# Optimization experiments

Measured on AMD Instinct MI355X. Metric: run time of the kernel, lower is better.

Reference implementation:

```python
import jax, jax.numpy as jnp
import numpy as np

D_MODEL = 1024
HEADS = 16
D_K = D_MODEL // HEADS  # 64


def setup_inputs() -> dict:
    key = jax.random.key(0)
    ks = jax.random.split(key, 9)
    B, S = 4, 2048
    values = jax.random.normal(ks[0], (B, S, D_MODEL), dtype=jnp.float32)
    keys = jax.random.normal(ks[1], (B, S, D_MODEL), dtype=jnp.float32)
    query = jax.random.normal(ks[2], (B, S, D_MODEL), dtype=jnp.float32)
    mask = jax.random.randint(ks[3], (1, 1, S, S), 0, 2, dtype=jnp.int32)
    # per-head projection weights (shared across heads), torch Linear layout (out, in)
    sc = 1.0 / np.sqrt(D_K)
    Wv = jax.random.uniform(ks[4], (D_K, D_K), jnp.float32, -sc, sc)
    Wk = jax.random.uniform(ks[5], (D_K, D_K), jnp.float32, -sc, sc)
    Wq = jax.random.uniform(ks[6], (D_K, D_K), jnp.float32, -sc, sc)
    so = 1.0 / np.sqrt(D_MODEL)
    Wo = jax.random.uniform(ks[7], (D_MODEL, D_MODEL), jnp.float32, -so, so)
    bo = jax.random.uniform(ks[8], (D_MODEL,), jnp.float32, -so, so)
    return {"values": values, "keys": keys, "query": query, "mask": mask,
            "Wv": Wv, "Wk": Wk, "Wq": Wq, "Wo": Wo, "bo": bo}


def reference(values, keys, query, mask, Wv, Wk, Wq, Wo, bo):
    n, q_len, d = query.shape
    v_len, k_len = values.shape[1], keys.shape[1]
    # reshape to (n, len, heads, d_k) and apply shared per-head linear (x @ W^T)
    v = values.reshape(n, v_len, HEADS, D_K) @ Wv.T
    k = keys.reshape(n, k_len, HEADS, D_K) @ Wk.T
    q = query.reshape(n, q_len, HEADS, D_K) @ Wq.T
    # scores: (n, h, q, k)
    scores = jnp.einsum('nqhd,nkhd->nhqk', q, k)
    scores = jnp.where(mask == 0, jnp.float32(-1e20), scores)
    attn = jax.nn.softmax(scores / jnp.sqrt(jnp.float32(D_K)), axis=3)
    out = jnp.einsum('nhqk,nkhd->nqhd', attn, v).reshape(n, q_len, HEADS * D_K)
    return out @ Wo.T + bo
```

## Files before the change

kernel.cpp:

```cpp
#include <hip/hip_runtime.h>

#define B 4
#define S 2048
#define H 16
#define DK 64
#define DM 1024
#define NTILES (S / 64)
#define QSCALE 0.18033688011112042f

typedef _Float16 half_t;
typedef __attribute__((ext_vector_type(8))) _Float16 half8v;
typedef __attribute__((ext_vector_type(2))) __fp16   fp16x2;
typedef __attribute__((ext_vector_type(4))) float    float4v;

__device__ __forceinline__ unsigned pkh(float lo, float hi) {
    union { fp16x2 h; unsigned u; } cvt;
    cvt.h = __builtin_amdgcn_cvt_pkrtz(lo, hi);
    return cvt.u;
}
__device__ __forceinline__ float fast_exp2(float x) {
#if __has_builtin(__builtin_amdgcn_exp2f)
    return __builtin_amdgcn_exp2f(x);
#else
    return __expf(x * 0.69314718055994531f);
#endif
}
__device__ __forceinline__ half8v cvt8h(float4 a, float4 b) {
    half8v r;
    r[0] = (half_t)a.x; r[1] = (half_t)a.y; r[2] = (half_t)a.z; r[3] = (half_t)a.w;
    r[4] = (half_t)b.x; r[5] = (half_t)b.y; r[6] = (half_t)b.z; r[7] = (half_t)b.w;
    return r;
}
__device__ __forceinline__ void gl2lds16(const void* g, void* l) {
    __builtin_amdgcn_global_load_lds(
        (const __attribute__((address_space(1))) unsigned int*)g,
        (__attribute__((address_space(3))) unsigned int*)l, 16, 0, 0);
}

#define MASK_BLOCKS (S * S / 256)
__global__ __launch_bounds__(256) void prep_kernel(
    const int* __restrict__ mask, unsigned long long* __restrict__ mp,
    const float* __restrict__ Wo, half_t* __restrict__ Wh)
{
    int bx = blockIdx.x;
    if (bx < MASK_BLOCKS) {
        int t = bx * 256 + threadIdx.x;
        int m = mask[t];
        unsigned long long b = __ballot(m != 0);
        if ((threadIdx.x & 63) == 0) mp[t >> 6] = b;
    } else {
        int t = ((bx - MASK_BLOCKS) * 256 + threadIdx.x) * 4;
        float4 wv = *(const float4*)(Wo + t);
        union { half_t h[4]; uint2 u; } cvt;
        cvt.h[0] = (half_t)wv.x; cvt.h[1] = (half_t)wv.y;
        cvt.h[2] = (half_t)wv.z; cvt.h[3] = (half_t)wv.w;
        *(uint2*)(Wh + t) = cvt.u;
    }
}

#define QSTR 72
__global__ __launch_bounds__(256) void qkv_proj_kernel(
    const float* __restrict__ xv, const float* __restrict__ xk, const float* __restrict__ xq,
    const float* __restrict__ Wv, const float* __restrict__ Wk, const float* __restrict__ Wq,
    half_t* __restrict__ vtw, half_t* __restrict__ kw, half_t* __restrict__ qw)
{
    __shared__ half_t Ls[64 * QSTR];

    const int y = blockIdx.y;
    const float* x; const float* W;
    if (y == 0)      { x = xv; W = Wv; }
    else if (y == 1) { x = xk; W = Wk; }
    else             { x = xq; W = Wq; }

    const int tid = threadIdx.x;
    const int w = tid >> 6, L = tid & 63, a = L & 15, g = L >> 4;
    const int bx  = blockIdx.x;
    const int st  = bx & 31;
    const int bh  = bx >> 5;
    const int b_  = bh >> 4, h = bh & 15;
    const int s0b = st * 64;

    half8v wF[4][2];
    #pragma unroll
    for (int t = 0; t < 4; ++t)
        #pragma unroll
        for (int c = 0; c < 2; ++c) {
            const float* wr = W + (size_t)(16 * t + a) * 64 + 32 * c + 8 * g;
            wF[t][c] = cvt8h(*(const float4*)wr, *(const float4*)(wr + 4));
        }

    const float* xr = x + ((size_t)(b_ * S) + s0b + 16 * w + a) * DM + h * 64 + 8 * g;
    half8v xF0 = cvt8h(*(const float4*)(xr),      *(const float4*)(xr + 4));
    half8v xF1 = cvt8h(*(const float4*)(xr + 32), *(const float4*)(xr + 36));

    const float4v z4 = {0.0f, 0.0f, 0.0f, 0.0f};

    if (y == 0) {
        const int c   = 16 * w + a;
        const int pos = 32 * (c >> 5) + 8 * ((c >> 2) & 3) + 4 * ((c >> 4) & 1) + (c & 3);
        #pragma unroll
        for (int mt = 0; mt < 4; ++mt) {
            float4v D = __builtin_amdgcn_mfma_f32_16x16x32_f16(wF[mt][0], xF0, z4, 0, 0, 0);
            D = __builtin_amdgcn_mfma_f32_16x16x32_f16(wF[mt][1], xF1, D, 0, 0, 0);
            #pragma unroll
            for (int r = 0; r < 4; ++r)
                Ls[(16 * mt + 4 * g + r) * QSTR + pos] = (half_t)D[r];
        }
    } else {
        const float scale = (y == 2) ? QSCALE : 1.0f;
        #pragma unroll
        for (int nt = 0; nt < 4; ++nt) {
            float4v D = __builtin_amdgcn_mfma_f32_16x16x32_f16(xF0, wF[nt][0], z4, 0, 0, 0);
            D = __builtin_amdgcn_mfma_f32_16x16x32_f16(xF1, wF[nt][1], D, 0, 0, 0);
            #pragma unroll
            for (int r = 0; r < 4; ++r)
                Ls[(16 * w + 4 * g + r) * QSTR + 16 * nt + a] = (half_t)(D[r] * scale);
        }
    }
    __syncthreads();

    const int row = tid >> 2;
    const int col = (tid & 3) * 16;
    uint4 v0 = *(const uint4*)&Ls[row * QSTR + col];
    uint4 v1 = *(const uint4*)&Ls[row * QSTR + col + 8];
    half_t* dst;
    if (y == 0)      dst = vtw + ((size_t)bh * 64 + row) * S + s0b + col;
    else {
        half_t* out = (y == 1) ? kw : qw;
        dst = out + ((size_t)bh * S + s0b + row) * 64 + col;
    }
    *(uint4*)dst = v0;
    *(uint4*)(dst + 8) = v1;
}

__global__ __launch_bounds__(512) void flash_attn_kernel(
    const half_t* __restrict__ q, const half_t* __restrict__ k,
    const half_t* __restrict__ vt, const unsigned long long* __restrict__ mp,
    half_t* __restrict__ att)
{
    __shared__ half_t KV[2][2][64 * 64];

    const int tid = threadIdx.x;
    const int w   = tid >> 6;
    const int L   = tid & 63;
    const int a   = L & 15;
    const int g   = L >> 4;
    const int bh  = blockIdx.x;
    const int b_  = bh >> 4, h = bh & 15;
    const int qs  = blockIdx.y * 256 + w * 32;

    const half_t* qb = q  + (size_t)bh * S * 64;
    const half_t* kb = k  + (size_t)bh * S * 64;
    const half_t* vb = vt + (size_t)bh * 64 * S;

    half8v qB[2][2];
    #pragma unroll
    for (int gq = 0; gq < 2; ++gq) {
        const half_t* qr = qb + (size_t)(qs + 16 * gq + a) * 64;
        qB[gq][0] = *(const half8v*)(qr +      g * 8);
        qB[gq][1] = *(const half8v*)(qr + 32 + g * 8);
    }

    const unsigned long long* mr[2];
    #pragma unroll
    for (int gq = 0; gq < 2; ++gq)
        mr[gq] = mp + (size_t)(qs + 16 * gq + a) * NTILES;

    const int p    = w * 64 + L;
    const int srow = p >> 3;
    const int schk = (p & 7) ^ (srow & 7);

    half8v ones;
    #pragma unroll
    for (int i = 0; i < 8; ++i) ones[i] = (half_t)1.0f;

    const float4v z4 = {0.0f, 0.0f, 0.0f, 0.0f};
    float4v o[2][4] = {{z4, z4, z4, z4}, {z4, z4, z4, z4}};
    float4v lD[2] = {z4, z4};

    gl2lds16(kb + (size_t)srow * 64 + schk * 8, &KV[0][0][w * 512]);
    gl2lds16(vb + (size_t)srow * S + schk * 8,  &KV[0][1][w * 512]);

    for (int kt = 0; kt < NTILES; ++kt) {
        const int cur = kt & 1;
        __syncthreads();

        if (kt + 1 < NTILES) {
            const int nk = kt + 1;
            gl2lds16(kb + ((size_t)(nk * 64 + srow)) * 64 + schk * 8,
                     &KV[cur ^ 1][0][w * 512]);
            gl2lds16(vb + (size_t)srow * S + nk * 64 + schk * 8,
                     &KV[cur ^ 1][1][w * 512]);
        }

        unsigned long long mw[2];
        #pragma unroll
        for (int gq = 0; gq < 2; ++gq) mw[gq] = mr[gq][kt];

        const half_t* Kb = &KV[cur][0][0];
        const half_t* Vb = &KV[cur][1][0];

        half8v kB[4][2], vA[4][2];
        #pragma unroll
        for (int nt = 0; nt < 4; ++nt)
            #pragma unroll
            for (int c = 0; c < 2; ++c) {
                const int off = ((16 * nt + a) * 8 + ((4 * c + g) ^ (a & 7))) * 8;
                kB[nt][c] = *(const half8v*)(Kb + off);
                vA[nt][c] = *(const half8v*)(Vb + off);
            }

        #pragma unroll
        for (int gq = 0; gq < 2; ++gq) {
            float4v st[4];
            #pragma unroll
            for (int nt = 0; nt < 4; ++nt) {
                st[nt] = __builtin_amdgcn_mfma_f32_16x16x32_f16(kB[nt][0], qB[gq][0], z4, 0, 0, 0);
                st[nt] = __builtin_amdgcn_mfma_f32_16x16x32_f16(kB[nt][1], qB[gq][1], st[nt], 0, 0, 0);
            }

            float e[4][4];
            #pragma unroll
            for (int nt = 0; nt < 4; ++nt) {
                unsigned bnt = (unsigned)(mw[gq] >> (16 * nt + 4 * g));
                #pragma unroll
                for (int r = 0; r < 4; ++r) {
                    float ee = fast_exp2(st[nt][r]);
                    e[nt][r] = ((bnt >> r) & 1u) ? ee : 0.0f;
                }
            }

            half8v pB[2];
            #pragma unroll
            for (int c = 0; c < 2; ++c) {
                union { unsigned u[4]; half8v hv; } cvt;
                cvt.u[0] = pkh(e[2*c  ][0], e[2*c  ][1]);
                cvt.u[1] = pkh(e[2*c  ][2], e[2*c  ][3]);
                cvt.u[2] = pkh(e[2*c+1][0], e[2*c+1][1]);
                cvt.u[3] = pkh(e[2*c+1][2], e[2*c+1][3]);
                pB[c] = cvt.hv;
            }

            #pragma unroll
            for (int nt = 0; nt < 4; ++nt) {
                o[gq][nt] = __builtin_amdgcn_mfma_f32_16x16x32_f16(vA[nt][0], pB[0], o[gq][nt], 0, 0, 0);
                o[gq][nt] = __builtin_amdgcn_mfma_f32_16x16x32_f16(vA[nt][1], pB[1], o[gq][nt], 0, 0, 0);
            }
            lD[gq] = __builtin_amdgcn_mfma_f32_16x16x32_f16(ones, pB[0], lD[gq], 0, 0, 0);
            lD[gq] = __builtin_amdgcn_mfma_f32_16x16x32_f16(ones, pB[1], lD[gq], 0, 0, 0);
        }
    }

    #pragma unroll
    for (int gq = 0; gq < 2; ++gq) {
        const float inv = 1.0f / lD[gq][0];
        const size_t row = (size_t)(b_ * S + qs + 16 * gq + a);
        #pragma unroll
        for (int nt = 0; nt < 4; ++nt) {
            union { unsigned u[2]; uint2 u2; } cvt;
            cvt.u[0] = pkh(o[gq][nt][0] * inv, o[gq][nt][1] * inv);
            cvt.u[1] = pkh(o[gq][nt][2] * inv, o[gq][nt][3] * inv);
            *(uint2*)(att + row * DM + h * 64 + 16 * nt + 4 * g) = cvt.u2;
        }
    }
}

__global__ __launch_bounds__(256, 2) void out_proj_kernel(
    const half_t* __restrict__ X, const half_t* __restrict__ Wh,
    const float* __restrict__ bo, float* __restrict__ out)
{
    __shared__ half_t SA[2][128 * 64], SB[2][128 * 64];

    const int tid = threadIdx.x;
    const int w = tid >> 6, L = tid & 63, a = L & 15, g = L >> 4;
    const int wm = w >> 1, wn = w & 1;
    const int r0 = blockIdx.x * 128;
    const int n0 = blockIdx.y * 128;

    int prow[4], pchk[4], pbase[4];
    #pragma unroll
    for (int i = 0; i < 4; ++i) {
        int p    = w * 256 + i * 64 + L;
        prow[i]  = p >> 3;
        pchk[i]  = (p & 7) ^ (prow[i] & 7);
        pbase[i] = (w * 256 + i * 64) * 8;
    }

    const float4v z4 = {0.0f, 0.0f, 0.0f, 0.0f};
    float4v acc[4][4];
    #pragma unroll
    for (int mt = 0; mt < 4; ++mt)
        #pragma unroll
        for (int nt = 0; nt < 4; ++nt) acc[mt][nt] = z4;

    #pragma unroll
    for (int i = 0; i < 4; ++i) {
        gl2lds16(X  + (size_t)(r0 + prow[i]) * DM + pchk[i] * 8, &SA[0][pbase[i]]);
        gl2lds16(Wh + (size_t)(n0 + prow[i]) * DM + pchk[i] * 8, &SB[0][pbase[i]]);
    }

    for (int kt = 0; kt < DM / 64; ++kt) {
        const int cur = kt & 1;
        __syncthreads();

        if (kt + 1 < DM / 64) {
            const int k0 = (kt + 1) * 64;
            #pragma unroll
            for (int i = 0; i < 4; ++i) {
                gl2lds16(X  + (size_t)(r0 + prow[i]) * DM + k0 + pchk[i] * 8, &SA[cur ^ 1][pbase[i]]);
                gl2lds16(Wh + (size_t)(n0 + prow[i]) * DM + k0 + pchk[i] * 8, &SB[cur ^ 1][pbase[i]]);
            }
        }

        half8v bF[4][2];
        #pragma unroll
        for (int nt = 0; nt < 4; ++nt)
            #pragma unroll
            for (int c = 0; c < 2; ++c) {
                const int rb  = 64 * wn + 16 * nt + a;
                const int off = (rb * 8 + ((4 * c + g) ^ (rb & 7))) * 8;
                bF[nt][c] = *(const half8v*)&SB[cur][off];
            }

        #pragma unroll
        for (int mt = 0; mt < 4; ++mt) {
            const int ra   = 64 * wm + 16 * mt + a;
            const int off0 = (ra * 8 + ((0 + g) ^ (ra & 7))) * 8;
            const int off1 = (ra * 8 + ((4 + g) ^ (ra & 7))) * 8;
            half8v a0 = *(const half8v*)&SA[cur][off0];
            half8v a1 = *(const half8v*)&SA[cur][off1];
            #pragma unroll
            for (int nt = 0; nt < 4; ++nt) {
                float4v acv = acc[mt][nt];
                acv = __builtin_amdgcn_mfma_f32_16x16x32_f16(a0, bF[nt][0], acv, 0, 0, 0);
                acv = __builtin_amdgcn_mfma_f32_16x16x32_f16(a1, bF[nt][1], acv, 0, 0, 0);
                acc[mt][nt] = acv;
            }
        }
    }

    #pragma unroll
    for (int mt = 0; mt < 4; ++mt) {
        const int m0 = r0 + 64 * wm + 16 * mt + 4 * g;
        #pragma unroll
        for (int nt = 0; nt < 4; ++nt) {
            const int n = n0 + 64 * wn + 16 * nt + a;
            const float bias = bo[n];
            #pragma unroll
            for (int r = 0; r < 4; ++r)
                out[(size_t)(m0 + r) * DM + n] = acc[mt][nt][r] + bias;
        }
    }
}

extern "C" void kernel_launch(void* const* d_in, const int* in_sizes, int n_in,
                              void* d_out, int out_size, void* d_ws, size_t ws_size,
                              hipStream_t stream) {
    (void)in_sizes; (void)n_in; (void)out_size; (void)ws_size;
    const float* values = (const float*)d_in[0];
    const float* keys   = (const float*)d_in[1];
    const float* query  = (const float*)d_in[2];
    const int*   mask   = (const int*)d_in[3];
    const float* Wv     = (const float*)d_in[4];
    const float* Wk     = (const float*)d_in[5];
    const float* Wq     = (const float*)d_in[6];
    const float* Wo     = (const float*)d_in[7];
    const float* bo     = (const float*)d_in[8];
    float* out = (float*)d_out;

    const size_t per = (size_t)B * H * S * DK;
    half_t* qw  = (half_t*)d_ws;
    half_t* kw  = qw + per;
    half_t* vtw = kw + per;
    unsigned long long* mp = (unsigned long long*)(vtw + per);
    half_t* atth = (half_t*)(mp + (size_t)S * S / 64);
    half_t* woh  = atth + per;

    prep_kernel<<<MASK_BLOCKS + DM * DM / 1024, 256, 0, stream>>>(mask, mp, Wo, woh);

    dim3 g1(B * H * (S / 64), 3);
    qkv_proj_kernel<<<g1, 256, 0, stream>>>(values, keys, query, Wv, Wk, Wq, vtw, kw, qw);

    dim3 g2(B * H, S / 256);
    flash_attn_kernel<<<g2, 512, 0, stream>>>(qw, kw, vtw, mp, atth);

    dim3 g3(B * S / 128, DM / 128);
    out_proj_kernel<<<g3, 256, 0, stream>>>(atth, woh, bo, out);
}
```

Before: 314.4 us.

## Deepen flash-attention K/V pipeline to four LDS buffers and stage mask via LDS

The flash attention loop moves from a double-buffered K/V tile ring to a four-slot ring with prefetch distance two. It uses explicit vmcnt waits and a raw s_barrier in place of a full __syncthreads. The bit-packed mask is stored transposed (tile-major) so each tile's mask words for a 256-row query block are contiguous. Those words are loaded asynchronously into LDS alongside K/V instead of as per-thread strided global loads. s_setprio is raised around the MFMA groups to favour matrix issue. LDS usage doubles, and the hand-tuned vmcnt counts depend on the exact number of outstanding loads.

```diff
diff --git a/kernel.cpp b/kernel.cpp
--- a/kernel.cpp
+++ b/kernel.cpp
@@ -36,10 +36,15 @@
         (const __attribute__((address_space(1))) unsigned int*)g,
         (__attribute__((address_space(3))) unsigned int*)l, 16, 0, 0);
 }
+__device__ __forceinline__ void gl2lds4(const void* g, void* l) {
+    __builtin_amdgcn_global_load_lds(
+        (const __attribute__((address_space(1))) unsigned int*)g,
+        (__attribute__((address_space(3))) unsigned int*)l, 4, 0, 0);
+}
 
 #define MASK_BLOCKS (S * S / 256)
 __global__ __launch_bounds__(256) void prep_kernel(
-    const int* __restrict__ mask, unsigned long long* __restrict__ mp,
+    const int* __restrict__ mask, unsigned long long* __restrict__ mpT,
     const float* __restrict__ Wo, half_t* __restrict__ Wh)
 {
     int bx = blockIdx.x;
@@ -47,7 +52,11 @@
         int t = bx * 256 + threadIdx.x;
         int m = mask[t];
         unsigned long long b = __ballot(m != 0);
-        if ((threadIdx.x & 63) == 0) mp[t >> 6] = b;
+        if ((threadIdx.x & 63) == 0) {
+            int row = t >> 11;
+            int kt  = (t & (S - 1)) >> 6;
+            mpT[(size_t)kt * S + row] = b;
+        }
     } else {
         int t = ((bx - MASK_BLOCKS) * 256 + threadIdx.x) * 4;
         float4 wv = *(const float4*)(Wo + t);
@@ -135,10 +144,11 @@
 
 __global__ __launch_bounds__(512) void flash_attn_kernel(
     const half_t* __restrict__ q, const half_t* __restrict__ k,
-    const half_t* __restrict__ vt, const unsigned long long* __restrict__ mp,
+    const half_t* __restrict__ vt, const unsigned long long* __restrict__ mpT,
     half_t* __restrict__ att)
 {
-    __shared__ half_t KV[2][2][64 * 64];
+    __shared__ half_t KV[4][2][64 * 64];
+    __shared__ unsigned long long Ms[4][256];
 
     const int tid = threadIdx.x;
     const int w   = tid >> 6;
@@ -147,11 +157,13 @@
     const int g   = L >> 4;
     const int bh  = blockIdx.x;
     const int b_  = bh >> 4, h = bh & 15;
-    const int qs  = blockIdx.y * 256 + w * 32;
+    const int qs0 = blockIdx.y * 256;
+    const int qs  = qs0 + w * 32;
 
     const half_t* qb = q  + (size_t)bh * S * 64;
     const half_t* kb = k  + (size_t)bh * S * 64;
     const half_t* vb = vt + (size_t)bh * 64 * S;
+    const unsigned long long* mq = mpT + qs0;
 
     half8v qB[2][2];
     #pragma unroll
@@ -160,15 +172,14 @@
         qB[gq][0] = *(const half8v*)(qr +      g * 8);
         qB[gq][1] = *(const half8v*)(qr + 32 + g * 8);
     }
-
-    const unsigned long long* mr[2];
-    #pragma unroll
-    for (int gq = 0; gq < 2; ++gq)
-        mr[gq] = mp + (size_t)(qs + 16 * gq + a) * NTILES;
+    asm volatile("s_waitcnt vmcnt(0)" ::: "memory");
+    __builtin_amdgcn_sched_barrier(0);
 
     const int p    = w * 64 + L;
     const int srow = p >> 3;
     const int schk = (p & 7) ^ (srow & 7);
+    const size_t kgo = (size_t)srow * 64 + schk * 8;
+    const size_t vgo = (size_t)srow * S  + schk * 8;
 
     half8v ones;
     #pragma unroll
@@ -178,27 +189,19 @@
     float4v o[2][4] = {{z4, z4, z4, z4}, {z4, z4, z4, z4}};
     float4v lD[2] = {z4, z4};
 
-    gl2lds16(kb + (size_t)srow * 64 + schk * 8, &KV[0][0][w * 512]);
-    gl2lds16(vb + (size_t)srow * S + schk * 8,  &KV[0][1][w * 512]);
-
-    for (int kt = 0; kt < NTILES; ++kt) {
-        const int cur = kt & 1;
-        __syncthreads();
-
-        if (kt + 1 < NTILES) {
-            const int nk = kt + 1;
-            gl2lds16(kb + ((size_t)(nk * 64 + srow)) * 64 + schk * 8,
-                     &KV[cur ^ 1][0][w * 512]);
-            gl2lds16(vb + (size_t)srow * S + nk * 64 + schk * 8,
-                     &KV[cur ^ 1][1][w * 512]);
-        }
-
-        unsigned long long mw[2];
-        #pragma unroll
-        for (int gq = 0; gq < 2; ++gq) mw[gq] = mr[gq][kt];
-
+    auto stage = [&](int kt2, int nb) {
+        gl2lds16(kb + (size_t)kt2 * 4096 + kgo, &KV[nb][0][w * 512]);
+        gl2lds16(vb + (size_t)kt2 * 64   + vgo, &KV[nb][1][w * 512]);
+        gl2lds4((const unsigned int*)(mq + (size_t)kt2 * S) + p, &Ms[nb][w * 32]);
+    };
+
+    auto compute = [&](int cur) {
         const half_t* Kb = &KV[cur][0][0];
         const half_t* Vb = &KV[cur][1][0];
+
+        unsigned long long mw[2];
+        mw[0] = Ms[cur][w * 32 +      a];
+        mw[1] = Ms[cur][w * 32 + 16 + a];
 
         half8v kB[4][2], vA[4][2];
         #pragma unroll
@@ -213,11 +216,13 @@
         #pragma unroll
         for (int gq = 0; gq < 2; ++gq) {
             float4v st[4];
+            __builtin_amdgcn_s_setprio(1);
             #pragma unroll
             for (int nt = 0; nt < 4; ++nt) {
                 st[nt] = __builtin_amdgcn_mfma_f32_16x16x32_f16(kB[nt][0], qB[gq][0], z4, 0, 0, 0);
                 st[nt] = __builtin_amdgcn_mfma_f32_16x16x32_f16(kB[nt][1], qB[gq][1], st[nt], 0, 0, 0);
             }
+            __builtin_amdgcn_s_setprio(0);
 
             float e[4][4];
             #pragma unroll
@@ -241,6 +246,7 @@
                 pB[c] = cvt.hv;
             }
 
+            __builtin_amdgcn_s_setprio(1);
             #pragma unroll
             for (int nt = 0; nt < 4; ++nt) {
                 o[gq][nt] = __builtin_amdgcn_mfma_f32_16x16x32_f16(vA[nt][0], pB[0], o[gq][nt], 0, 0, 0);
@@ -248,7 +254,26 @@
             }
             lD[gq] = __builtin_amdgcn_mfma_f32_16x16x32_f16(ones, pB[0], lD[gq], 0, 0, 0);
             lD[gq] = __builtin_amdgcn_mfma_f32_16x16x32_f16(ones, pB[1], lD[gq], 0, 0, 0);
-        }
+            __builtin_amdgcn_s_setprio(0);
+        }
+    };
+
+    stage(0, 0);
+    stage(1, 1);
+    __builtin_amdgcn_sched_barrier(0);
+
+    for (int kt = 0; kt < NTILES; ++kt) {
+        const int cur = kt & 3;
+        __builtin_amdgcn_sched_barrier(0);
+        if (kt < NTILES - 1) asm volatile("s_waitcnt vmcnt(3)" ::: "memory");
+        else                 asm volatile("s_waitcnt vmcnt(0)" ::: "memory");
+        __builtin_amdgcn_s_barrier();
+        __builtin_amdgcn_sched_barrier(0);
+        if (kt + 2 < NTILES) {
+            stage(kt + 2, (kt + 2) & 3);
+            __builtin_amdgcn_sched_barrier(0);
+        }
+        compute(cur);
     }
 
     #pragma unroll
@@ -372,17 +397,17 @@
     half_t* qw  = (half_t*)d_ws;
     half_t* kw  = qw + per;
     half_t* vtw = kw + per;
-    unsigned long long* mp = (unsigned long long*)(vtw + per);
-    half_t* atth = (half_t*)(mp + (size_t)S * S / 64);
+    unsigned long long* mpT = (unsigned long long*)(vtw + per);
+    half_t* atth = (half_t*)(mpT + (size_t)S * S / 64);
     half_t* woh  = atth + per;
 
-    prep_kernel<<<MASK_BLOCKS + DM * DM / 1024, 256, 0, stream>>>(mask, mp, Wo, woh);
+    prep_kernel<<<MASK_BLOCKS + DM * DM / 1024, 256, 0, stream>>>(mask, mpT, Wo, woh);
 
     dim3 g1(B * H * (S / 64), 3);
     qkv_proj_kernel<<<g1, 256, 0, stream>>>(values, keys, query, Wv, Wk, Wq, vtw, kw, qw);
 
     dim3 g2(B * H, S / 256);
-    flash_attn_kernel<<<g2, 512, 0, stream>>>(qw, kw, vtw, mp, atth);
+    flash_attn_kernel<<<g2, 512, 0, stream>>>(qw, kw, vtw, mpT, atth);
 
     dim3 g3(B * S / 128, DM / 128);
     out_proj_kernel<<<g3, 256, 0, stream>>>(atth, woh, bo, out);
```

Result: slower. 330.1 us (+5.0%).

## Fold mask packing and Wo conversion into QKV projection; prioritise MFMA waves

Applied to the files above, without the earlier changes.

Removes the separate prep kernel and runs mask bit-packing and Wo fp16 conversion as an extra grid row (y==3) of the QKV projection kernel, with each block packing 2048 mask entries and the first 1024 blocks converting Wo. This saves one kernel launch and lets the prep work overlap with the projection. It also raises wave priority around the MFMA sections of the flash attention loop so matrix instructions are issued ahead of the exp and softmax arithmetic. The extra grid row launches 2048 more blocks, and the priority hints may not change scheduling much.

```diff
diff --git a/kernel.cpp b/kernel.cpp
--- a/kernel.cpp
+++ b/kernel.cpp
@@ -37,44 +37,45 @@
         (__attribute__((address_space(3))) unsigned int*)l, 16, 0, 0);
 }
 
-#define MASK_BLOCKS (S * S / 256)
-__global__ __launch_bounds__(256) void prep_kernel(
-    const int* __restrict__ mask, unsigned long long* __restrict__ mp,
-    const float* __restrict__ Wo, half_t* __restrict__ Wh)
-{
-    int bx = blockIdx.x;
-    if (bx < MASK_BLOCKS) {
-        int t = bx * 256 + threadIdx.x;
-        int m = mask[t];
-        unsigned long long b = __ballot(m != 0);
-        if ((threadIdx.x & 63) == 0) mp[t >> 6] = b;
-    } else {
-        int t = ((bx - MASK_BLOCKS) * 256 + threadIdx.x) * 4;
-        float4 wv = *(const float4*)(Wo + t);
-        union { half_t h[4]; uint2 u; } cvt;
-        cvt.h[0] = (half_t)wv.x; cvt.h[1] = (half_t)wv.y;
-        cvt.h[2] = (half_t)wv.z; cvt.h[3] = (half_t)wv.w;
-        *(uint2*)(Wh + t) = cvt.u;
-    }
-}
-
 #define QSTR 72
 __global__ __launch_bounds__(256) void qkv_proj_kernel(
     const float* __restrict__ xv, const float* __restrict__ xk, const float* __restrict__ xq,
     const float* __restrict__ Wv, const float* __restrict__ Wk, const float* __restrict__ Wq,
-    half_t* __restrict__ vtw, half_t* __restrict__ kw, half_t* __restrict__ qw)
+    half_t* __restrict__ vtw, half_t* __restrict__ kw, half_t* __restrict__ qw,
+    const int* __restrict__ mask, unsigned long long* __restrict__ mp,
+    const float* __restrict__ Wo, half_t* __restrict__ Wh)
 {
     __shared__ half_t Ls[64 * QSTR];
 
-    const int y = blockIdx.y;
+    const int y   = blockIdx.y;
+    const int tid = threadIdx.x;
+    const int bx  = blockIdx.x;
+
+    if (y == 3) {
+        const int base = bx * 2048;
+        #pragma unroll
+        for (int it = 0; it < 8; ++it) {
+            int t = base + it * 256 + tid;
+            unsigned long long bb = __ballot(mask[t] != 0);
+            if ((tid & 63) == 0) mp[t >> 6] = bb;
+        }
+        if (bx < DM * DM / 1024) {
+            int t = (bx * 256 + tid) * 4;
+            float4 wv = *(const float4*)(Wo + t);
+            union { half_t h[4]; uint2 u; } cvt;
+            cvt.h[0] = (half_t)wv.x; cvt.h[1] = (half_t)wv.y;
+            cvt.h[2] = (half_t)wv.z; cvt.h[3] = (half_t)wv.w;
+            *(uint2*)(Wh + t) = cvt.u;
+        }
+        return;
+    }
+
     const float* x; const float* W;
     if (y == 0)      { x = xv; W = Wv; }
     else if (y == 1) { x = xk; W = Wk; }
     else             { x = xq; W = Wq; }
 
-    const int tid = threadIdx.x;
     const int w = tid >> 6, L = tid & 63, a = L & 15, g = L >> 4;
-    const int bx  = blockIdx.x;
     const int st  = bx & 31;
     const int bh  = bx >> 5;
     const int b_  = bh >> 4, h = bh & 15;
@@ -213,11 +214,13 @@
         #pragma unroll
         for (int gq = 0; gq < 2; ++gq) {
             float4v st[4];
+            __builtin_amdgcn_s_setprio(1);
             #pragma unroll
             for (int nt = 0; nt < 4; ++nt) {
                 st[nt] = __builtin_amdgcn_mfma_f32_16x16x32_f16(kB[nt][0], qB[gq][0], z4, 0, 0, 0);
                 st[nt] = __builtin_amdgcn_mfma_f32_16x16x32_f16(kB[nt][1], qB[gq][1], st[nt], 0, 0, 0);
             }
+            __builtin_amdgcn_s_setprio(0);
 
             float e[4][4];
             #pragma unroll
@@ -241,6 +244,7 @@
                 pB[c] = cvt.hv;
             }
 
+            __builtin_amdgcn_s_setprio(1);
             #pragma unroll
             for (int nt = 0; nt < 4; ++nt) {
                 o[gq][nt] = __builtin_amdgcn_mfma_f32_16x16x32_f16(vA[nt][0], pB[0], o[gq][nt], 0, 0, 0);
@@ -248,6 +252,7 @@
             }
             lD[gq] = __builtin_amdgcn_mfma_f32_16x16x32_f16(ones, pB[0], lD[gq], 0, 0, 0);
             lD[gq] = __builtin_amdgcn_mfma_f32_16x16x32_f16(ones, pB[1], lD[gq], 0, 0, 0);
+            __builtin_amdgcn_s_setprio(0);
         }
     }
 
@@ -376,10 +381,9 @@
     half_t* atth = (half_t*)(mp + (size_t)S * S / 64);
     half_t* woh  = atth + per;
 
-    prep_kernel<<<MASK_BLOCKS + DM * DM / 1024, 256, 0, stream>>>(mask, mp, Wo, woh);
-
-    dim3 g1(B * H * (S / 64), 3);
-    qkv_proj_kernel<<<g1, 256, 0, stream>>>(values, keys, query, Wv, Wk, Wq, vtw, kw, qw);
+    dim3 g1(B * H * (S / 64), 4);
+    qkv_proj_kernel<<<g1, 256, 0, stream>>>(values, keys, query, Wv, Wk, Wq,
+                                            vtw, kw, qw, mask, mp, Wo, woh);
 
     dim3 g2(B * H, S / 256);
     flash_attn_kernel<<<g2, 512, 0, stream>>>(qw, kw, vtw, mp, atth);
```

Result: slower. 326.1 us (+3.7%).
